# Kernel tuning notes

Hardware: AMD Instinct MI355X
Metric: run time of the kernel (lower is better)

## Reference

```python
import jax, jax.numpy as jnp
import numpy as np

D_MODEL = 256
SCALE = 1.0 / float(np.sqrt(D_MODEL))


def setup_inputs() -> dict:
    key = jax.random.key(0)
    kq, kk, kv, km = jax.random.split(key, 4)
    B, S, D = 16, 2048, D_MODEL
    q = jax.random.normal(kq, (B, S, D), dtype=jnp.float32)
    k = jax.random.normal(kk, (B, S, D), dtype=jnp.float32)
    v = jax.random.normal(kv, (B, S, D), dtype=jnp.float32)
    mask = jax.random.randint(km, (1, S, S), 0, 2, dtype=jnp.int32)
    return {"q": q, "k": k, "v": v, "mask": mask}


def reference(q, k, v, mask):
    # scores: [B, S, S] = q @ k^T * scale
    scores = jnp.einsum("bqd,bkd->bqk", q, k) * SCALE
    scores = jnp.where(mask == 0, -jnp.inf, scores)
    attn_weights = jax.nn.softmax(scores, axis=-1)
    output = jnp.einsum("bqk,bkd->bqd", attn_weights, v)
    return (output, attn_weights)
```

## Files before the change

kernel.cpp:

```cpp
#include <hip/hip_runtime.h>
#include <hip/hip_bf16.h>
#include <stdint.h>


#define B_ 16
#define S_ 2048
#define D_ 256
#define SCALE_ 0.0625f

typedef __attribute__((ext_vector_type(8))) short bf16x8;
typedef __attribute__((ext_vector_type(4))) float f32x4;

__device__ __forceinline__ uint16_t f2bf(float f) {
  uint32_t u = __float_as_uint(f);
  u += 0x7fffu + ((u >> 16) & 1u);
  return (uint16_t)(u >> 16);
}

typedef __attribute__((address_space(3))) uint32_t lds_u32;
typedef __attribute__((address_space(1))) const uint32_t glb_u32;
__device__ __forceinline__ void gload_lds16(const void* g, void* l) {
  __builtin_amdgcn_global_load_lds((glb_u32*)g, (lds_u32*)l, 16, 0, 0);
}

__global__ void k_convert(const float* __restrict__ src, uint16_t* __restrict__ dst) {
  const int t = blockIdx.x * blockDim.x + threadIdx.x;
  const float4* s = (const float4*)src + (size_t)t * 2;
  float4 a = s[0], b = s[1];
  ushort4 lo = { f2bf(a.x), f2bf(a.y), f2bf(a.z), f2bf(a.w) };
  ushort4 hi = { f2bf(b.x), f2bf(b.y), f2bf(b.z), f2bf(b.w) };
  ((ushort4*)dst)[(size_t)t * 2]     = lo;
  ((ushort4*)dst)[(size_t)t * 2 + 1] = hi;
}

__global__ void k_transpose(const float* __restrict__ V, uint16_t* __restrict__ Vt) {
  __shared__ float tile[64][68];
  const int b = blockIdx.z, kv0 = blockIdx.x * 64, d0 = blockIdx.y * 64;
  const int t = threadIdx.x;
  {
    const int r = t >> 2, c = (t & 3) * 16;
    const float4* src = (const float4*)(V + ((size_t)b * S_ + kv0 + r) * D_ + d0 + c);
    float4 x0 = src[0], x1 = src[1], x2 = src[2], x3 = src[3];
    *(float4*)&tile[r][c]      = x0;
    *(float4*)&tile[r][c + 4]  = x1;
    *(float4*)&tile[r][c + 8]  = x2;
    *(float4*)&tile[r][c + 12] = x3;
  }
  __syncthreads();
  {
    const int dl = t >> 2, c = (t & 3) * 16;
    uint16_t o[16];
#pragma unroll
    for (int i = 0; i < 16; ++i) o[i] = f2bf(tile[c + i][dl]);
    uint16_t* dst = Vt + ((size_t)b * D_ + d0 + dl) * S_ + kv0 + c;
#pragma unroll
    for (int i = 0; i < 4; ++i) {
      ushort4 v4 = { o[4*i], o[4*i+1], o[4*i+2], o[4*i+3] };
      *(ushort4*)(dst + 4*i) = v4;
    }
  }
}

__global__ void k_maskpack(const int* __restrict__ mask, unsigned long long* __restrict__ Mb) {
  const int wid  = blockIdx.x * 4 + (threadIdx.x >> 6);
  const int lane = threadIdx.x & 63;
  const int row = wid >> 5, w64 = wid & 31;
  const int m = mask[(size_t)row * S_ + w64 * 64 + lane];
  unsigned long long bits = __ballot(m != 0);
  if (lane == 0) Mb[row * 32 + w64] = bits;
}

__global__ __launch_bounds__(256, 2) void k_attn(
    const float* __restrict__ Q, const uint16_t* __restrict__ Kb,
    const unsigned long long* __restrict__ Mb,
    float* __restrict__ E, float* __restrict__ Winv) {
  __shared__ uint16_t Ks[128 * 256];
  const int b = blockIdx.y, q0 = blockIdx.x * 64;
  const int tid = threadIdx.x, w = tid >> 6, lane = tid & 63;
  const int wq = w >> 1, wkv = w & 1;
  const int l15 = lane & 15, lq = lane >> 4;
  const int qbase = q0 + wq * 32;

  bf16x8 aq[2][8];
#pragma unroll
  for (int qt = 0; qt < 2; ++qt) {
    const float* qrow = Q + ((size_t)b * S_ + qbase + qt * 16 + l15) * D_;
#pragma unroll
    for (int dc = 0; dc < 8; ++dc) {
      const float4* p = (const float4*)(qrow + dc * 32 + lq * 8);
      float4 x = p[0], y = p[1];
      union { bf16x8 v; uint16_t u[8]; } fr;
      fr.u[0] = f2bf(x.x); fr.u[1] = f2bf(x.y); fr.u[2] = f2bf(x.z); fr.u[3] = f2bf(x.w);
      fr.u[4] = f2bf(y.x); fr.u[5] = f2bf(y.y); fr.u[6] = f2bf(y.z); fr.u[7] = f2bf(y.w);
      aq[qt][dc] = fr.v;
    }
  }

  float rowpart[2][4] = {{0.f,0.f,0.f,0.f},{0.f,0.f,0.f,0.f}};

  for (int kvt = 0; kvt < 16; ++kvt) {
    const int kvb = kvt * 128;
    __syncthreads();
    {
      const uint16_t* tbase = Kb + ((size_t)b * S_ + kvb) * D_;
#pragma unroll
      for (int it = 0; it < 16; ++it) {
        const int s = (it * 4 + w) * 64 + lane;
        const int r = s >> 5, c = s & 31;
        const int g = (c & ~7) | ((c ^ r) & 7);
        gload_lds16(tbase + (size_t)r * D_ + g * 8, &Ks[(it * 4 + w) * 64 * 8]);
      }
    }
    __syncthreads();

    f32x4 acc[2][4];
#pragma unroll
    for (int qt = 0; qt < 2; ++qt)
#pragma unroll
      for (int kt = 0; kt < 4; ++kt) acc[qt][kt] = 0.f;

#pragma unroll
    for (int dc = 0; dc < 8; ++dc) {
      bf16x8 bk[4];
#pragma unroll
      for (int kt = 0; kt < 4; ++kt) {
        const int kvl = wkv * 64 + kt * 16 + l15;
        const int g = dc * 4 + lq;
        const int gs = (g & ~7) | ((g ^ kvl) & 7);
        bk[kt] = *(const bf16x8*)&Ks[(kvl * 32 + gs) * 8];
      }
#pragma unroll
      for (int qt = 0; qt < 2; ++qt)
#pragma unroll
        for (int kt = 0; kt < 4; ++kt)
          acc[qt][kt] = __builtin_amdgcn_mfma_f32_16x16x32_bf16(
              aq[qt][dc], bk[kt], acc[qt][kt], 0, 0, 0);
    }

#pragma unroll
    for (int qt = 0; qt < 2; ++qt) {
#pragma unroll
      for (int r = 0; r < 4; ++r) {
        const int row = qbase + qt * 16 + lq * 4 + r;
        const unsigned long long mw = Mb[row * 32 + kvt * 2 + wkv];
        float* erow = E + (size_t)b * S_ * S_ + (size_t)row * S_ + kvb + wkv * 64 + l15;
#pragma unroll
        for (int kt = 0; kt < 4; ++kt) {
          const float sc = acc[qt][kt][r] * SCALE_;
          const int bit = kt * 16 + l15;
          const float e = ((mw >> bit) & 1ull) ? __expf(sc) : 0.0f;
          rowpart[qt][r] += e;
          erow[kt * 16] = e;
        }
      }
    }
  }

#pragma unroll
  for (int qt = 0; qt < 2; ++qt)
#pragma unroll
    for (int r = 0; r < 4; ++r) {
      float v = rowpart[qt][r];
      v += __shfl_xor(v, 1); v += __shfl_xor(v, 2);
      v += __shfl_xor(v, 4); v += __shfl_xor(v, 8);
      rowpart[qt][r] = v;
    }
  __syncthreads();
  float* red = (float*)(void*)Ks;
  if (l15 == 0) {
#pragma unroll
    for (int qt = 0; qt < 2; ++qt)
#pragma unroll
      for (int r = 0; r < 4; ++r) {
        const int rl = wq * 32 + qt * 16 + lq * 4 + r;
        red[wkv * 64 + rl] = rowpart[qt][r];
      }
  }
  __syncthreads();
  if (wkv == 0 && l15 == 0) {
#pragma unroll
    for (int qt = 0; qt < 2; ++qt)
#pragma unroll
      for (int r = 0; r < 4; ++r) {
        const int rl = wq * 32 + qt * 16 + lq * 4 + r;
        Winv[(size_t)b * S_ + q0 + rl] = 1.0f / (red[rl] + red[64 + rl]);
      }
  }
}

__global__ __launch_bounds__(256, 2) void k_out(
    float* __restrict__ attn, const uint16_t* __restrict__ Vt,
    const float* __restrict__ Winv, float* __restrict__ O) {
  __shared__ uint16_t As[64 * 64];
  __shared__ uint16_t Vs[256 * 64];
  const int b = blockIdx.y, q0 = blockIdx.x * 64;
  const int tid = threadIdx.x, w = tid >> 6, lane = tid & 63;
  const int l15 = lane & 15, lq = lane >> 4;
  const int srow = tid >> 2, scol = (tid & 3) * 16;
  const float inv_r = Winv[(size_t)b * S_ + q0 + srow];

  f32x4 acc[4][4];
#pragma unroll
  for (int qt = 0; qt < 4; ++qt)
#pragma unroll
    for (int dt = 0; dt < 4; ++dt) acc[qt][dt] = 0.f;

  for (int kvt = 0; kvt < 32; ++kvt) {
    const int kvb = kvt * 64;
    __syncthreads();
    {
      const uint16_t* tbase = Vt + (size_t)b * D_ * S_ + kvb;
#pragma unroll
      for (int it = 0; it < 8; ++it) {
        const int s = (it * 4 + w) * 64 + lane;
        const int d = s >> 3, c = s & 7;
        const int g = c ^ (d & 7);
        gload_lds16(tbase + (size_t)d * S_ + g * 8, &Vs[(it * 4 + w) * 64 * 8]);
      }
    }
    {
      float* ap = attn + ((size_t)b * S_ + q0 + srow) * S_ + kvb + scol;
      float4 a0 = ((const float4*)ap)[0], a1 = ((const float4*)ap)[1];
      float4 a2 = ((const float4*)ap)[2], a3 = ((const float4*)ap)[3];
      a0.x *= inv_r; a0.y *= inv_r; a0.z *= inv_r; a0.w *= inv_r;
      a1.x *= inv_r; a1.y *= inv_r; a1.z *= inv_r; a1.w *= inv_r;
      a2.x *= inv_r; a2.y *= inv_r; a2.z *= inv_r; a2.w *= inv_r;
      a3.x *= inv_r; a3.y *= inv_r; a3.z *= inv_r; a3.w *= inv_r;
      ((float4*)ap)[0] = a0; ((float4*)ap)[1] = a1;
      ((float4*)ap)[2] = a2; ((float4*)ap)[3] = a3;
      union { uint4 u; uint16_t h[8]; } g0, g1;
      g0.h[0] = f2bf(a0.x); g0.h[1] = f2bf(a0.y); g0.h[2] = f2bf(a0.z); g0.h[3] = f2bf(a0.w);
      g0.h[4] = f2bf(a1.x); g0.h[5] = f2bf(a1.y); g0.h[6] = f2bf(a1.z); g0.h[7] = f2bf(a1.w);
      g1.h[0] = f2bf(a2.x); g1.h[1] = f2bf(a2.y); g1.h[2] = f2bf(a2.z); g1.h[3] = f2bf(a2.w);
      g1.h[4] = f2bf(a3.x); g1.h[5] = f2bf(a3.y); g1.h[6] = f2bf(a3.z); g1.h[7] = f2bf(a3.w);
      const int gc = (tid & 3) * 2;
      *(uint4*)&As[(srow * 8 + (gc ^ (srow & 7))) * 8]       = g0.u;
      *(uint4*)&As[(srow * 8 + ((gc + 1) ^ (srow & 7))) * 8] = g1.u;
    }
    __syncthreads();

#pragma unroll
    for (int kc = 0; kc < 2; ++kc) {
      bf16x8 af[4], bv[4];
      const int g = kc * 4 + lq;
#pragma unroll
      for (int qt = 0; qt < 4; ++qt) {
        const int ql = qt * 16 + l15;
        af[qt] = *(const bf16x8*)&As[(ql * 8 + (g ^ (ql & 7))) * 8];
      }
#pragma unroll
      for (int dt = 0; dt < 4; ++dt) {
        const int dl = w * 64 + dt * 16 + l15;
        bv[dt] = *(const bf16x8*)&Vs[(dl * 8 + (g ^ (dl & 7))) * 8];
      }
#pragma unroll
      for (int qt = 0; qt < 4; ++qt)
#pragma unroll
        for (int dt = 0; dt < 4; ++dt)
          acc[qt][dt] = __builtin_amdgcn_mfma_f32_16x16x32_bf16(af[qt], bv[dt], acc[qt][dt], 0, 0, 0);
    }
  }

#pragma unroll
  for (int qt = 0; qt < 4; ++qt)
#pragma unroll
    for (int dt = 0; dt < 4; ++dt)
#pragma unroll
      for (int r = 0; r < 4; ++r)
        O[((size_t)b * S_ + q0 + qt * 16 + lq * 4 + r) * D_ +
          w * 64 + dt * 16 + l15] = acc[qt][dt][r];
}

extern "C" void kernel_launch(void* const* d_in, const int* in_sizes, int n_in,
                              void* d_out, int out_size, void* d_ws, size_t ws_size,
                              hipStream_t stream) {
  const float* q = (const float*)d_in[0];
  const float* k = (const float*)d_in[1];
  const float* v = (const float*)d_in[2];
  const int* mask = (const int*)d_in[3];

  float* out  = (float*)d_out;
  float* attn = out + (size_t)B_ * S_ * D_;

  uint16_t* Kb = (uint16_t*)d_ws;
  uint16_t* Vt = Kb + (size_t)B_ * S_ * D_;
  unsigned long long* Mb = (unsigned long long*)(Vt + (size_t)B_ * S_ * D_);
  float* Winv = (float*)(Mb + (size_t)S_ * 32);

  k_convert<<<dim3(2048), dim3(512), 0, stream>>>(k, Kb);
  k_transpose<<<dim3(32, 4, 16), dim3(256), 0, stream>>>(v, Vt);
  k_maskpack<<<dim3(16384), dim3(256), 0, stream>>>(mask, Mb);
  k_attn<<<dim3(32, 16), dim3(256), 0, stream>>>(q, Kb, Mb, attn, Winv);
  k_out<<<dim3(32, 16), dim3(256), 0, stream>>>(attn, Vt, Winv, out);
}
```

Measured before the change: 579.4 us.

## Fuse PV matmul into score kernel and normalize attention in separate pass

The P·V product now runs inside the score kernel: unnormalized exp values go to LDS as bf16 and are multiplied against V read straight from global memory, and the output is scaled by the inverse row sum at the end. A light k_norm kernel then rescales the stored attention weights. This drops the separate k_out pass, which read the full attention matrix, rescaled it and wrote it back while restaging V. K staging is moved so the next tile loads during the PV phase, and MFMA blocks get raised wave priority. In exchange the fused kernel carries more accumulator registers and reads V uncached from global memory, which could lower occupancy.

```diff
diff --git a/kernel.cpp b/kernel.cpp
--- a/kernel.cpp
+++ b/kernel.cpp
@@ -72,9 +72,10 @@
 
 __global__ __launch_bounds__(256, 2) void k_attn(
     const float* __restrict__ Q, const uint16_t* __restrict__ Kb,
-    const unsigned long long* __restrict__ Mb,
-    float* __restrict__ E, float* __restrict__ Winv) {
+    const unsigned long long* __restrict__ Mb, const uint16_t* __restrict__ Vt,
+    float* __restrict__ E, float* __restrict__ Winv, float* __restrict__ O) {
   __shared__ uint16_t Ks[128 * 256];
+  __shared__ uint16_t Ps[64 * 128];
   const int b = blockIdx.y, q0 = blockIdx.x * 64;
   const int tid = threadIdx.x, w = tid >> 6, lane = tid & 63;
   const int wq = w >> 1, wkv = w & 1;
@@ -96,21 +97,34 @@
     }
   }
 
+  const uint16_t* vtd[4];
+#pragma unroll
+  for (int dt = 0; dt < 4; ++dt)
+    vtd[dt] = Vt + ((size_t)b * D_ + w * 64 + dt * 16 + l15) * S_;
+
+  f32x4 accO[4][4];
+#pragma unroll
+  for (int qt = 0; qt < 4; ++qt)
+#pragma unroll
+    for (int dt = 0; dt < 4; ++dt) accO[qt][dt] = 0.f;
+
   float rowpart[2][4] = {{0.f,0.f,0.f,0.f},{0.f,0.f,0.f,0.f}};
+
+  auto stage = [&](int kvb_s) {
+    const uint16_t* tbase = Kb + ((size_t)b * S_ + kvb_s) * D_;
+#pragma unroll
+    for (int it = 0; it < 16; ++it) {
+      const int s = (it * 4 + w) * 64 + lane;
+      const int r = s >> 5, c = s & 31;
+      const int g = (c & ~7) | ((c ^ r) & 7);
+      gload_lds16(tbase + (size_t)r * D_ + g * 8, &Ks[(it * 4 + w) * 64 * 8]);
+    }
+  };
+
+  stage(0);
 
   for (int kvt = 0; kvt < 16; ++kvt) {
     const int kvb = kvt * 128;
-    __syncthreads();
-    {
-      const uint16_t* tbase = Kb + ((size_t)b * S_ + kvb) * D_;
-#pragma unroll
-      for (int it = 0; it < 16; ++it) {
-        const int s = (it * 4 + w) * 64 + lane;
-        const int r = s >> 5, c = s & 31;
-        const int g = (c & ~7) | ((c ^ r) & 7);
-        gload_lds16(tbase + (size_t)r * D_ + g * 8, &Ks[(it * 4 + w) * 64 * 8]);
-      }
-    }
     __syncthreads();
 
     f32x4 acc[2][4];
@@ -129,20 +143,23 @@
         const int gs = (g & ~7) | ((g ^ kvl) & 7);
         bk[kt] = *(const bf16x8*)&Ks[(kvl * 32 + gs) * 8];
       }
+      __builtin_amdgcn_s_setprio(1);
 #pragma unroll
       for (int qt = 0; qt < 2; ++qt)
 #pragma unroll
         for (int kt = 0; kt < 4; ++kt)
           acc[qt][kt] = __builtin_amdgcn_mfma_f32_16x16x32_bf16(
               aq[qt][dc], bk[kt], acc[qt][kt], 0, 0, 0);
+      __builtin_amdgcn_s_setprio(0);
     }
 
 #pragma unroll
     for (int qt = 0; qt < 2; ++qt) {
 #pragma unroll
       for (int r = 0; r < 4; ++r) {
-        const int row = qbase + qt * 16 + lq * 4 + r;
-        const unsigned long long mw = Mb[row * 32 + kvt * 2 + wkv];
+        const int qloc = wq * 32 + qt * 16 + lq * 4 + r;
+        const int row = q0 + qloc;
+        const unsigned long long mw = Mb[(size_t)row * 32 + kvt * 2 + wkv];
         float* erow = E + (size_t)b * S_ * S_ + (size_t)row * S_ + kvb + wkv * 64 + l15;
 #pragma unroll
         for (int kt = 0; kt < 4; ++kt) {
@@ -151,116 +168,74 @@
           const float e = ((mw >> bit) & 1ull) ? __expf(sc) : 0.0f;
           rowpart[qt][r] += e;
           erow[kt * 16] = e;
+          const int kvloc = wkv * 64 + kt * 16 + l15;
+          *(uint16_t*)((char*)Ps +
+              (((qloc * 256) + kvloc * 2) ^ ((qloc & 7) << 4))) = f2bf(e);
         }
       }
     }
+    __syncthreads();
+
+    if (kvt + 1 < 16) stage(kvb + 128);
+
+#pragma unroll
+    for (int kc = 0; kc < 4; ++kc) {
+      bf16x8 af[4], bv[4];
+#pragma unroll
+      for (int qt = 0; qt < 4; ++qt) {
+        const int qr = qt * 16 + l15;
+        af[qt] = *(const bf16x8*)((const char*)Ps +
+                   (((qr * 256) + (kc * 64 + lq * 16)) ^ ((qr & 7) << 4)));
+      }
+#pragma unroll
+      for (int dt = 0; dt < 4; ++dt)
+        bv[dt] = *(const bf16x8*)(vtd[dt] + kvb + kc * 32 + lq * 8);
+      __builtin_amdgcn_s_setprio(1);
+#pragma unroll
+      for (int qt = 0; qt < 4; ++qt)
+#pragma unroll
+        for (int dt = 0; dt < 4; ++dt)
+          accO[qt][dt] = __builtin_amdgcn_mfma_f32_16x16x32_bf16(
+              af[qt], bv[dt], accO[qt][dt], 0, 0, 0);
+      __builtin_amdgcn_s_setprio(0);
+    }
   }
 
 #pragma unroll
   for (int qt = 0; qt < 2; ++qt)
 #pragma unroll
     for (int r = 0; r < 4; ++r) {
-      float v = rowpart[qt][r];
-      v += __shfl_xor(v, 1); v += __shfl_xor(v, 2);
-      v += __shfl_xor(v, 4); v += __shfl_xor(v, 8);
-      rowpart[qt][r] = v;
+      float vs = rowpart[qt][r];
+      vs += __shfl_xor(vs, 1); vs += __shfl_xor(vs, 2);
+      vs += __shfl_xor(vs, 4); vs += __shfl_xor(vs, 8);
+      rowpart[qt][r] = vs;
     }
   __syncthreads();
-  float* red = (float*)(void*)Ks;
+  float* red = (float*)(void*)Ps;
   if (l15 == 0) {
 #pragma unroll
     for (int qt = 0; qt < 2; ++qt)
 #pragma unroll
-      for (int r = 0; r < 4; ++r) {
-        const int rl = wq * 32 + qt * 16 + lq * 4 + r;
-        red[wkv * 64 + rl] = rowpart[qt][r];
-      }
+      for (int r = 0; r < 4; ++r)
+        red[wkv * 64 + wq * 32 + qt * 16 + lq * 4 + r] = rowpart[qt][r];
   }
   __syncthreads();
-  if (wkv == 0 && l15 == 0) {
-#pragma unroll
-    for (int qt = 0; qt < 2; ++qt)
-#pragma unroll
-      for (int r = 0; r < 4; ++r) {
-        const int rl = wq * 32 + qt * 16 + lq * 4 + r;
-        Winv[(size_t)b * S_ + q0 + rl] = 1.0f / (red[rl] + red[64 + rl]);
-      }
-  }
-}
-
-__global__ __launch_bounds__(256, 2) void k_out(
-    float* __restrict__ attn, const uint16_t* __restrict__ Vt,
-    const float* __restrict__ Winv, float* __restrict__ O) {
-  __shared__ uint16_t As[64 * 64];
-  __shared__ uint16_t Vs[256 * 64];
-  const int b = blockIdx.y, q0 = blockIdx.x * 64;
-  const int tid = threadIdx.x, w = tid >> 6, lane = tid & 63;
-  const int l15 = lane & 15, lq = lane >> 4;
-  const int srow = tid >> 2, scol = (tid & 3) * 16;
-  const float inv_r = Winv[(size_t)b * S_ + q0 + srow];
-
-  f32x4 acc[4][4];
+
+  float inv[4][4];
 #pragma unroll
   for (int qt = 0; qt < 4; ++qt)
 #pragma unroll
-    for (int dt = 0; dt < 4; ++dt) acc[qt][dt] = 0.f;
-
-  for (int kvt = 0; kvt < 32; ++kvt) {
-    const int kvb = kvt * 64;
-    __syncthreads();
-    {
-      const uint16_t* tbase = Vt + (size_t)b * D_ * S_ + kvb;
-#pragma unroll
-      for (int it = 0; it < 8; ++it) {
-        const int s = (it * 4 + w) * 64 + lane;
-        const int d = s >> 3, c = s & 7;
-        const int g = c ^ (d & 7);
-        gload_lds16(tbase + (size_t)d * S_ + g * 8, &Vs[(it * 4 + w) * 64 * 8]);
-      }
-    }
-    {
-      float* ap = attn + ((size_t)b * S_ + q0 + srow) * S_ + kvb + scol;
-      float4 a0 = ((const float4*)ap)[0], a1 = ((const float4*)ap)[1];
-      float4 a2 = ((const float4*)ap)[2], a3 = ((const float4*)ap)[3];
-      a0.x *= inv_r; a0.y *= inv_r; a0.z *= inv_r; a0.w *= inv_r;
-      a1.x *= inv_r; a1.y *= inv_r; a1.z *= inv_r; a1.w *= inv_r;
-      a2.x *= inv_r; a2.y *= inv_r; a2.z *= inv_r; a2.w *= inv_r;
-      a3.x *= inv_r; a3.y *= inv_r; a3.z *= inv_r; a3.w *= inv_r;
-      ((float4*)ap)[0] = a0; ((float4*)ap)[1] = a1;
-      ((float4*)ap)[2] = a2; ((float4*)ap)[3] = a3;
-      union { uint4 u; uint16_t h[8]; } g0, g1;
-      g0.h[0] = f2bf(a0.x); g0.h[1] = f2bf(a0.y); g0.h[2] = f2bf(a0.z); g0.h[3] = f2bf(a0.w);
-      g0.h[4] = f2bf(a1.x); g0.h[5] = f2bf(a1.y); g0.h[6] = f2bf(a1.z); g0.h[7] = f2bf(a1.w);
-      g1.h[0] = f2bf(a2.x); g1.h[1] = f2bf(a2.y); g1.h[2] = f2bf(a2.z); g1.h[3] = f2bf(a2.w);
-      g1.h[4] = f2bf(a3.x); g1.h[5] = f2bf(a3.y); g1.h[6] = f2bf(a3.z); g1.h[7] = f2bf(a3.w);
-      const int gc = (tid & 3) * 2;
-      *(uint4*)&As[(srow * 8 + (gc ^ (srow & 7))) * 8]       = g0.u;
-      *(uint4*)&As[(srow * 8 + ((gc + 1) ^ (srow & 7))) * 8] = g1.u;
-    }
-    __syncthreads();
-
-#pragma unroll
-    for (int kc = 0; kc < 2; ++kc) {
-      bf16x8 af[4], bv[4];
-      const int g = kc * 4 + lq;
-#pragma unroll
-      for (int qt = 0; qt < 4; ++qt) {
-        const int ql = qt * 16 + l15;
-        af[qt] = *(const bf16x8*)&As[(ql * 8 + (g ^ (ql & 7))) * 8];
-      }
-#pragma unroll
-      for (int dt = 0; dt < 4; ++dt) {
-        const int dl = w * 64 + dt * 16 + l15;
-        bv[dt] = *(const bf16x8*)&Vs[(dl * 8 + (g ^ (dl & 7))) * 8];
-      }
-#pragma unroll
-      for (int qt = 0; qt < 4; ++qt)
-#pragma unroll
-        for (int dt = 0; dt < 4; ++dt)
-          acc[qt][dt] = __builtin_amdgcn_mfma_f32_16x16x32_bf16(af[qt], bv[dt], acc[qt][dt], 0, 0, 0);
-    }
-  }
-
+    for (int r = 0; r < 4; ++r) {
+      const int rl = qt * 16 + lq * 4 + r;
+      inv[qt][r] = 1.0f / (red[rl] + red[64 + rl]);
+    }
+  if (w == 0 && l15 == 0) {
+#pragma unroll
+    for (int qt = 0; qt < 4; ++qt)
+#pragma unroll
+      for (int r = 0; r < 4; ++r)
+        Winv[(size_t)b * S_ + q0 + qt * 16 + lq * 4 + r] = inv[qt][r];
+  }
 #pragma unroll
   for (int qt = 0; qt < 4; ++qt)
 #pragma unroll
@@ -268,7 +243,21 @@
 #pragma unroll
       for (int r = 0; r < 4; ++r)
         O[((size_t)b * S_ + q0 + qt * 16 + lq * 4 + r) * D_ +
-          w * 64 + dt * 16 + l15] = acc[qt][dt][r];
+          w * 64 + dt * 16 + l15] = accO[qt][dt][r] * inv[qt][r];
+}
+
+__global__ __launch_bounds__(256) void k_norm(float* __restrict__ attn,
+                                              const float* __restrict__ Winv) {
+  const int row0 = blockIdx.x * 4;
+  float4* p = (float4*)(attn + (size_t)row0 * S_);
+#pragma unroll
+  for (int it = 0; it < 8; ++it) {
+    const int idx = it * 256 + threadIdx.x;
+    const float inv = Winv[row0 + (idx >> 9)];
+    float4 a = p[idx];
+    a.x *= inv; a.y *= inv; a.z *= inv; a.w *= inv;
+    p[idx] = a;
+  }
 }
 
 extern "C" void kernel_launch(void* const* d_in, const int* in_sizes, int n_in,
@@ -290,6 +279,6 @@
   k_convert<<<dim3(2048), dim3(512), 0, stream>>>(k, Kb);
   k_transpose<<<dim3(32, 4, 16), dim3(256), 0, stream>>>(v, Vt);
   k_maskpack<<<dim3(16384), dim3(256), 0, stream>>>(mask, Mb);
-  k_attn<<<dim3(32, 16), dim3(256), 0, stream>>>(q, Kb, Mb, attn, Winv);
-  k_out<<<dim3(32, 16), dim3(256), 0, stream>>>(attn, Vt, Winv, out);
-}
+  k_attn<<<dim3(32, 16), dim3(256), 0, stream>>>(q, Kb, Mb, Vt, attn, Winv, out);
+  k_norm<<<dim3(16 * S_ / 4), dim3(256), 0, stream>>>(attn, Winv);
+}
```

Result: slower. 750.0 us (+29.5%).

## Double-buffer K/V and attention tiles, swizzle block order, add nontemporal accesses

Applied to the files above, without the earlier changes.

Both attention kernels now double-buffer their LDS tiles. The global-to-LDS load for the next tile is issued right after the barrier, so it overlaps the MFMA work on the current tile. In k_out, the load of the next unnormalized attention row chunk is also prefetched into registers and scaled after the current MFMAs. k_attn switches to 64-wide KV tiles, and the grid is flattened with a block-index swizzle that remaps work to blocks. MFMA sections are wrapped in s_setprio, and the large attention-matrix traffic uses nontemporal loads and stores to cut cache pollution, at the cost of more LDS and registers per block.

```diff
diff --git a/kernel.cpp b/kernel.cpp
--- a/kernel.cpp
+++ b/kernel.cpp
@@ -74,8 +74,10 @@
     const float* __restrict__ Q, const uint16_t* __restrict__ Kb,
     const unsigned long long* __restrict__ Mb,
     float* __restrict__ E, float* __restrict__ Winv) {
-  __shared__ uint16_t Ks[128 * 256];
-  const int b = blockIdx.y, q0 = blockIdx.x * 64;
+  __shared__ uint16_t Ks[2][64 * 256];
+  const int bid = blockIdx.x;
+  const int swz = (bid & 7) * 64 + (bid >> 3);
+  const int b = swz >> 5, q0 = (swz & 31) * 64;
   const int tid = threadIdx.x, w = tid >> 6, lane = tid & 63;
   const int wq = w >> 1, wkv = w & 1;
   const int l15 = lane & 15, lq = lane >> 4;
@@ -98,59 +100,66 @@
 
   float rowpart[2][4] = {{0.f,0.f,0.f,0.f},{0.f,0.f,0.f,0.f}};
 
-  for (int kvt = 0; kvt < 16; ++kvt) {
-    const int kvb = kvt * 128;
+  auto stage = [&](int t) {
+    const uint16_t* tbase = Kb + ((size_t)b * S_ + t * 64) * D_;
+    uint16_t* lbase = Ks[t & 1];
+#pragma unroll
+    for (int it = 0; it < 8; ++it) {
+      const int s = (it * 4 + w) * 64 + lane;
+      const int r = s >> 5, c = s & 31;
+      const int g = (c & ~7) | ((c ^ r) & 7);
+      gload_lds16(tbase + (size_t)r * D_ + g * 8, lbase + (size_t)(it * 4 + w) * 64 * 8);
+    }
+  };
+
+  stage(0);
+
+  for (int t = 0; t < 32; ++t) {
     __syncthreads();
-    {
-      const uint16_t* tbase = Kb + ((size_t)b * S_ + kvb) * D_;
-#pragma unroll
-      for (int it = 0; it < 16; ++it) {
-        const int s = (it * 4 + w) * 64 + lane;
-        const int r = s >> 5, c = s & 31;
-        const int g = (c & ~7) | ((c ^ r) & 7);
-        gload_lds16(tbase + (size_t)r * D_ + g * 8, &Ks[(it * 4 + w) * 64 * 8]);
-      }
-    }
-    __syncthreads();
-
-    f32x4 acc[2][4];
+    if (t + 1 < 32) stage(t + 1);
+    const uint16_t* kbuf = Ks[t & 1];
+
+    f32x4 acc[2][2];
 #pragma unroll
     for (int qt = 0; qt < 2; ++qt)
 #pragma unroll
-      for (int kt = 0; kt < 4; ++kt) acc[qt][kt] = 0.f;
+      for (int kt = 0; kt < 2; ++kt) acc[qt][kt] = 0.f;
 
 #pragma unroll
     for (int dc = 0; dc < 8; ++dc) {
-      bf16x8 bk[4];
-#pragma unroll
-      for (int kt = 0; kt < 4; ++kt) {
-        const int kvl = wkv * 64 + kt * 16 + l15;
+      bf16x8 bk[2];
+#pragma unroll
+      for (int kt = 0; kt < 2; ++kt) {
+        const int kvl = wkv * 32 + kt * 16 + l15;
         const int g = dc * 4 + lq;
         const int gs = (g & ~7) | ((g ^ kvl) & 7);
-        bk[kt] = *(const bf16x8*)&Ks[(kvl * 32 + gs) * 8];
-      }
+        bk[kt] = *(const bf16x8*)&kbuf[(kvl * 32 + gs) * 8];
+      }
+      __builtin_amdgcn_s_setprio(1);
 #pragma unroll
       for (int qt = 0; qt < 2; ++qt)
 #pragma unroll
-        for (int kt = 0; kt < 4; ++kt)
+        for (int kt = 0; kt < 2; ++kt)
           acc[qt][kt] = __builtin_amdgcn_mfma_f32_16x16x32_bf16(
               aq[qt][dc], bk[kt], acc[qt][kt], 0, 0, 0);
-    }
-
+      __builtin_amdgcn_s_setprio(0);
+    }
+
+    const int kvb = t * 64;
 #pragma unroll
     for (int qt = 0; qt < 2; ++qt) {
 #pragma unroll
       for (int r = 0; r < 4; ++r) {
         const int row = qbase + qt * 16 + lq * 4 + r;
-        const unsigned long long mw = Mb[row * 32 + kvt * 2 + wkv];
-        float* erow = E + (size_t)b * S_ * S_ + (size_t)row * S_ + kvb + wkv * 64 + l15;
-#pragma unroll
-        for (int kt = 0; kt < 4; ++kt) {
+        const unsigned long long mw = Mb[(size_t)row * 32 + t];
+        float* erow = E + (size_t)b * S_ * S_ + (size_t)row * S_ + kvb + wkv * 32 + l15;
+#pragma unroll
+        for (int kt = 0; kt < 2; ++kt) {
           const float sc = acc[qt][kt][r] * SCALE_;
-          const int bit = kt * 16 + l15;
+          const int bit = wkv * 32 + kt * 16 + l15;
           const float e = ((mw >> bit) & 1ull) ? __expf(sc) : 0.0f;
           rowpart[qt][r] += e;
-          erow[kt * 16] = e;
+          __builtin_nontemporal_store(e, erow + kt * 16);
         }
       }
     }
@@ -160,21 +169,18 @@
   for (int qt = 0; qt < 2; ++qt)
 #pragma unroll
     for (int r = 0; r < 4; ++r) {
-      float v = rowpart[qt][r];
-      v += __shfl_xor(v, 1); v += __shfl_xor(v, 2);
-      v += __shfl_xor(v, 4); v += __shfl_xor(v, 8);
-      rowpart[qt][r] = v;
-    }
-  __syncthreads();
-  float* red = (float*)(void*)Ks;
+      float vs = rowpart[qt][r];
+      vs += __shfl_xor(vs, 1); vs += __shfl_xor(vs, 2);
+      vs += __shfl_xor(vs, 4); vs += __shfl_xor(vs, 8);
+      rowpart[qt][r] = vs;
+    }
+  float* red = (float*)(void*)Ks[0];
   if (l15 == 0) {
 #pragma unroll
     for (int qt = 0; qt < 2; ++qt)
 #pragma unroll
-      for (int r = 0; r < 4; ++r) {
-        const int rl = wq * 32 + qt * 16 + lq * 4 + r;
-        red[wkv * 64 + rl] = rowpart[qt][r];
-      }
+      for (int r = 0; r < 4; ++r)
+        red[wkv * 64 + wq * 32 + qt * 16 + lq * 4 + r] = rowpart[qt][r];
   }
   __syncthreads();
   if (wkv == 0 && l15 == 0) {
@@ -191,13 +197,16 @@
 __global__ __launch_bounds__(256, 2) void k_out(
     float* __restrict__ attn, const uint16_t* __restrict__ Vt,
     const float* __restrict__ Winv, float* __restrict__ O) {
-  __shared__ uint16_t As[64 * 64];
-  __shared__ uint16_t Vs[256 * 64];
-  const int b = blockIdx.y, q0 = blockIdx.x * 64;
+  __shared__ uint16_t As[2][64 * 64];
+  __shared__ uint16_t Vs[2][256 * 64];
+  const int bid = blockIdx.x;
+  const int swz = (bid & 7) * 64 + (bid >> 3);
+  const int b = swz >> 5, q0 = (swz & 31) * 64;
   const int tid = threadIdx.x, w = tid >> 6, lane = tid & 63;
   const int l15 = lane & 15, lq = lane >> 4;
-  const int srow = tid >> 2, scol = (tid & 3) * 16;
+  const int srow = tid >> 2;
   const float inv_r = Winv[(size_t)b * S_ + q0 + srow];
+  float* aprow = attn + ((size_t)b * S_ + q0 + srow) * S_ + (tid & 3) * 16;
 
   f32x4 acc[4][4];
 #pragma unroll
@@ -205,39 +214,53 @@
 #pragma unroll
     for (int dt = 0; dt < 4; ++dt) acc[qt][dt] = 0.f;
 
-  for (int kvt = 0; kvt < 32; ++kvt) {
-    const int kvb = kvt * 64;
+  f32x4 e0, e1, e2, e3;
+
+  auto stageV = [&](int t) {
+    const uint16_t* tbase = Vt + (size_t)b * D_ * S_ + t * 64;
+    uint16_t* lbase = Vs[t & 1];
+#pragma unroll
+    for (int it = 0; it < 8; ++it) {
+      const int s = (it * 4 + w) * 64 + lane;
+      const int d = s >> 3, c = s & 7;
+      const int g = c ^ (d & 7);
+      gload_lds16(tbase + (size_t)d * S_ + g * 8, lbase + (size_t)(it * 4 + w) * 64 * 8);
+    }
+  };
+  auto loadE = [&](int t) {
+    const f32x4* ap = (const f32x4*)(aprow + (size_t)t * 64);
+    e0 = __builtin_nontemporal_load(ap);
+    e1 = __builtin_nontemporal_load(ap + 1);
+    e2 = __builtin_nontemporal_load(ap + 2);
+    e3 = __builtin_nontemporal_load(ap + 3);
+  };
+  auto procE = [&](int t) {
+    e0 *= inv_r; e1 *= inv_r; e2 *= inv_r; e3 *= inv_r;
+    f32x4* ap = (f32x4*)(aprow + (size_t)t * 64);
+    __builtin_nontemporal_store(e0, ap);
+    __builtin_nontemporal_store(e1, ap + 1);
+    __builtin_nontemporal_store(e2, ap + 2);
+    __builtin_nontemporal_store(e3, ap + 3);
+    union { uint4 u; uint16_t h[8]; } g0, g1;
+    g0.h[0] = f2bf(e0[0]); g0.h[1] = f2bf(e0[1]); g0.h[2] = f2bf(e0[2]); g0.h[3] = f2bf(e0[3]);
+    g0.h[4] = f2bf(e1[0]); g0.h[5] = f2bf(e1[1]); g0.h[6] = f2bf(e1[2]); g0.h[7] = f2bf(e1[3]);
+    g1.h[0] = f2bf(e2[0]); g1.h[1] = f2bf(e2[1]); g1.h[2] = f2bf(e2[2]); g1.h[3] = f2bf(e2[3]);
+    g1.h[4] = f2bf(e3[0]); g1.h[5] = f2bf(e3[1]); g1.h[6] = f2bf(e3[2]); g1.h[7] = f2bf(e3[3]);
+    const int gc = (tid & 3) * 2;
+    uint16_t* abuf = As[t & 1];
+    *(uint4*)&abuf[(srow * 8 + (gc ^ (srow & 7))) * 8]       = g0.u;
+    *(uint4*)&abuf[(srow * 8 + ((gc + 1) ^ (srow & 7))) * 8] = g1.u;
+  };
+
+  stageV(0);
+  loadE(0);
+  procE(0);
+
+  for (int t = 0; t < 32; ++t) {
     __syncthreads();
-    {
-      const uint16_t* tbase = Vt + (size_t)b * D_ * S_ + kvb;
-#pragma unroll
-      for (int it = 0; it < 8; ++it) {
-        const int s = (it * 4 + w) * 64 + lane;
-        const int d = s >> 3, c = s & 7;
-        const int g = c ^ (d & 7);
-        gload_lds16(tbase + (size_t)d * S_ + g * 8, &Vs[(it * 4 + w) * 64 * 8]);
-      }
-    }
-    {
-      float* ap = attn + ((size_t)b * S_ + q0 + srow) * S_ + kvb + scol;
-      float4 a0 = ((const float4*)ap)[0], a1 = ((const float4*)ap)[1];
-      float4 a2 = ((const float4*)ap)[2], a3 = ((const float4*)ap)[3];
-      a0.x *= inv_r; a0.y *= inv_r; a0.z *= inv_r; a0.w *= inv_r;
-      a1.x *= inv_r; a1.y *= inv_r; a1.z *= inv_r; a1.w *= inv_r;
-      a2.x *= inv_r; a2.y *= inv_r; a2.z *= inv_r; a2.w *= inv_r;
-      a3.x *= inv_r; a3.y *= inv_r; a3.z *= inv_r; a3.w *= inv_r;
-      ((float4*)ap)[0] = a0; ((float4*)ap)[1] = a1;
-      ((float4*)ap)[2] = a2; ((float4*)ap)[3] = a3;
-      union { uint4 u; uint16_t h[8]; } g0, g1;
-      g0.h[0] = f2bf(a0.x); g0.h[1] = f2bf(a0.y); g0.h[2] = f2bf(a0.z); g0.h[3] = f2bf(a0.w);
-      g0.h[4] = f2bf(a1.x); g0.h[5] = f2bf(a1.y); g0.h[6] = f2bf(a1.z); g0.h[7] = f2bf(a1.w);
-      g1.h[0] = f2bf(a2.x); g1.h[1] = f2bf(a2.y); g1.h[2] = f2bf(a2.z); g1.h[3] = f2bf(a2.w);
-      g1.h[4] = f2bf(a3.x); g1.h[5] = f2bf(a3.y); g1.h[6] = f2bf(a3.z); g1.h[7] = f2bf(a3.w);
-      const int gc = (tid & 3) * 2;
-      *(uint4*)&As[(srow * 8 + (gc ^ (srow & 7))) * 8]       = g0.u;
-      *(uint4*)&As[(srow * 8 + ((gc + 1) ^ (srow & 7))) * 8] = g1.u;
-    }
-    __syncthreads();
+    if (t + 1 < 32) { stageV(t + 1); loadE(t + 1); }
+    const uint16_t* abuf = As[t & 1];
+    const uint16_t* vbuf = Vs[t & 1];
 
 #pragma unroll
     for (int kc = 0; kc < 2; ++kc) {
@@ -246,19 +269,22 @@
 #pragma unroll
       for (int qt = 0; qt < 4; ++qt) {
         const int ql = qt * 16 + l15;
-        af[qt] = *(const bf16x8*)&As[(ql * 8 + (g ^ (ql & 7))) * 8];
+        af[qt] = *(const bf16x8*)&abuf[(ql * 8 + (g ^ (ql & 7))) * 8];
       }
 #pragma unroll
       for (int dt = 0; dt < 4; ++dt) {
         const int dl = w * 64 + dt * 16 + l15;
-        bv[dt] = *(const bf16x8*)&Vs[(dl * 8 + (g ^ (dl & 7))) * 8];
-      }
+        bv[dt] = *(const bf16x8*)&vbuf[(dl * 8 + (g ^ (dl & 7))) * 8];
+      }
+      __builtin_amdgcn_s_setprio(1);
 #pragma unroll
       for (int qt = 0; qt < 4; ++qt)
 #pragma unroll
         for (int dt = 0; dt < 4; ++dt)
           acc[qt][dt] = __builtin_amdgcn_mfma_f32_16x16x32_bf16(af[qt], bv[dt], acc[qt][dt], 0, 0, 0);
-    }
+      __builtin_amdgcn_s_setprio(0);
+    }
+    if (t + 1 < 32) procE(t + 1);
   }
 
 #pragma unroll
@@ -290,6 +316,6 @@
   k_convert<<<dim3(2048), dim3(512), 0, stream>>>(k, Kb);
   k_transpose<<<dim3(32, 4, 16), dim3(256), 0, stream>>>(v, Vt);
   k_maskpack<<<dim3(16384), dim3(256), 0, stream>>>(mask, Mb);
-  k_attn<<<dim3(32, 16), dim3(256), 0, stream>>>(q, Kb, Mb, attn, Winv);
-  k_out<<<dim3(32, 16), dim3(256), 0, stream>>>(attn, Vt, Winv, out);
-}
+  k_attn<<<dim3(512), dim3(256), 0, stream>>>(q, Kb, Mb, attn, Winv);
+  k_out<<<dim3(512), dim3(256), 0, stream>>>(attn, Vt, Winv, out);
+}
```

Measured after the change: 631.7 us. +9.0%, slower.
